# Optimization experiments

Measured on AMD Instinct MI355X. Metric: run time of the kernel, lower is better.

Reference implementation:

```python
import jax, jax.numpy as jnp
import numpy as np

K = 8                     # block_size
EPS_MIN, EPS_MAX = 2.0, 15.0
ROUND_M, ROUND_N = 10, 10
TEMP = 50.0               # round_temperature
INIT_QUALITY = 90

STD_LUMA = np.array([[16,11,10,16,24,40,51,61],[12,12,14,19,26,58,60,55],[14,13,16,24,40,57,69,56],[14,17,22,29,51,87,80,62],[18,22,37,56,68,109,103,77],[24,35,55,64,81,104,113,92],[49,64,78,87,103,121,120,101],[72,92,95,98,112,100,103,99]], dtype=np.float32)
STD_CHROMA = np.array([[17,18,24,47,99,99,99,99],[18,21,26,66,99,99,99,99],[24,26,56,99,99,99,99,99],[47,66,99,99,99,99,99,99],[99,99,99,99,99,99,99,99],[99,99,99,99,99,99,99,99],[99,99,99,99,99,99,99,99],[99,99,99,99,99,99,99,99]], dtype=np.float32)

def _quality_to_table(base, quality):
    scale = 5000.0 / quality if quality < 50 else 200.0 - 2.0 * quality
    return np.clip(np.floor((base * scale + 50.0) / 100.0), 1.0, 255.0).astype(np.float32)

def _dct_matrix(k):
    n = np.arange(k)
    mat = np.sqrt(2.0 / k) * np.cos((2 * n[None, :] + 1) * n[:, None] * np.pi / (2.0 * k))
    mat[0, :] = np.sqrt(1.0 / k)
    return jnp.asarray(mat, dtype=jnp.float32)

DCT = _dct_matrix(K)  # (K, K)

def _soft_round(x):
    # Differentiable staircase round over integer range [-M, N]:
    # round(x) ~= -M + sum_{k=-M}^{N-1} sigmoid(T * (x - k - 0.5))
    ks = jnp.arange(-ROUND_M, ROUND_N, dtype=jnp.float32)
    return -float(ROUND_M) + jnp.sum(jax.nn.sigmoid(TEMP * (x[..., None] - ks - 0.5)), axis=-1)

def setup_inputs() -> dict:
    key = jax.random.key(0)
    k_img, _ = jax.random.split(key)
    images = jax.random.uniform(k_img, (8, 3, 512, 512), dtype=jnp.float32)
    q_y = jnp.asarray(_quality_to_table(STD_LUMA, INIT_QUALITY))
    q_c = jnp.asarray(_quality_to_table(STD_CHROMA, INIT_QUALITY))
    return {"images": images, "q_y": q_y, "q_c": q_c}

def reference(images, q_y, q_c):
    x = jnp.clip(images, 0.0, 1.0)
    B, C, H, W = x.shape  # H, W are multiples of K (no padding needed)
    # RGB -> YCbCr
    r, g, b = x[:, 0:1], x[:, 1:2], x[:, 2:3]
    y  =  0.299 * r + 0.587 * g + 0.114 * b
    cb = -0.168736 * r - 0.331264 * g + 0.5 * b + 0.5
    cr =  0.5 * r - 0.418688 * g - 0.081312 * b + 0.5
    yc = jnp.concatenate([y, cb, cr], axis=1)
    # blockwise layout: (B, C, H/K, W/K, K, K)
    blocks = yc.reshape(B, C, H // K, K, W // K, K).transpose(0, 1, 2, 4, 3, 5)
    # 2D DCT per original code convention: coef = D @ X @ D (note: NOT D X D^T)
    coef = jnp.einsum('ij,bcuvjk,kl->bcuvil', DCT, blocks, DCT)
    # clamped learnable quant tables; chroma table shared by Cb and Cr
    qy = jnp.clip(q_y, EPS_MIN, EPS_MAX)
    qc = jnp.clip(q_c, EPS_MIN, EPS_MAX)
    qt = jnp.stack([qy, qc, qc])[None, :, None, None]  # (1,3,1,1,K,K)
    quant = _soft_round(coef / qt) * qt
    # 2D IDCT: rec = D^T @ X @ D^T (inverse of the above convention)
    rec = jnp.einsum('ji,bcuvjk,lk->bcuvil', DCT, quant, DCT)
    rec = rec.transpose(0, 1, 2, 4, 3, 5).reshape(B, C, H, W)
    # YCbCr -> RGB
    y2, cb2, cr2 = rec[:, 0:1], rec[:, 1:2] - 0.5, rec[:, 2:3] - 0.5
    r2 = y2 + 1.402 * cr2
    g2 = y2 - 0.344136 * cb2 - 0.714136 * cr2
    b2 = y2 + 1.772 * cb2
    out = jnp.concatenate([r2, g2, b2], axis=1)
    return jnp.clip(out, 0.0, 1.0)
```

## Files before the change

### kernel.cpp

```cpp
#include <hip/hip_runtime.h>
#include <math.h>

namespace {

constexpr int LDSS = 76;

struct DctMat {
  float d[8][8];
  constexpr DctMat() : d{} {
    const float CT[17] = {
        1.0f, 0.9807852804032304f, 0.9238795325112867f, 0.8314696123025452f,
        0.7071067811865476f, 0.5555702330196022f, 0.3826834323650898f,
        0.19509032201612825f, 0.0f, -0.19509032201612825f,
        -0.3826834323650898f, -0.5555702330196022f, -0.7071067811865476f,
        -0.8314696123025452f, -0.9238795325112867f, -0.9807852804032304f,
        -1.0f};
    for (int i = 0; i < 8; ++i)
      for (int j = 0; j < 8; ++j) {
        if (i == 0) {
          d[i][j] = 0.35355339059327373f;
        } else {
          int m = ((2 * j + 1) * i) % 32;
          if (m > 16) m = 32 - m;
          d[i][j] = 0.5f * CT[m];
        }
      }
  }
};
constexpr DctMat DM{};

template <bool TRANSPOSED>
__device__ __forceinline__ void mul8(const float (&a)[8], float (&t)[8]) {
#pragma unroll
  for (int i = 0; i < 8; ++i) {
    float s = 0.0f;
#pragma unroll
    for (int j = 0; j < 8; ++j) {
      s = fmaf(a[j], TRANSPOSED ? DM.d[j][i] : DM.d[i][j], s);
    }
    t[i] = s;
  }
}

__device__ __forceinline__ void transpose3(float (&T)[3][8], float* lds, int blk,
                                           int r) {
#pragma unroll
  for (int c = 0; c < 3; ++c) {
    float* lp = lds + (c * 8 + blk) * LDSS;
#pragma unroll
    for (int j = 0; j < 8; ++j) lp[j * 8 + r] = T[c][j];
  }
  __syncthreads();
#pragma unroll
  for (int c = 0; c < 3; ++c) {
    const float* lp = lds + (c * 8 + blk) * LDSS + r * 8;
    float4 v0 = *reinterpret_cast<const float4*>(lp);
    float4 v1 = *reinterpret_cast<const float4*>(lp + 4);
    T[c][0] = v0.x; T[c][1] = v0.y; T[c][2] = v0.z; T[c][3] = v0.w;
    T[c][4] = v1.x; T[c][5] = v1.y; T[c][6] = v1.z; T[c][7] = v1.w;
  }
  __syncthreads();
}

__device__ __forceinline__ void quant8(float (&a)[8], const float (&q)[8]) {
#pragma unroll
  for (int i = 0; i < 8; ++i) {
    float qv = q[i];
    float x = a[i] * __builtin_amdgcn_rcpf(qv);
    float kc = floorf(x);
    kc = fmaxf(-10.0f, fminf(9.0f, kc));
    float arg = 50.0f * (x - kc - 0.5f);
    float e = __expf(-arg);
    float sr = kc + __builtin_amdgcn_rcpf(1.0f + e);
    a[i] = sr * qv;
  }
}

__device__ __forceinline__ void load8(const float* __restrict__ p, float (&a)[8]) {
  float4 v0 = *reinterpret_cast<const float4*>(p);
  float4 v1 = *reinterpret_cast<const float4*>(p + 4);
  a[0] = v0.x; a[1] = v0.y; a[2] = v0.z; a[3] = v0.w;
  a[4] = v1.x; a[5] = v1.y; a[6] = v1.z; a[7] = v1.w;
}

__device__ __forceinline__ void store8(float* __restrict__ p, const float (&a)[8]) {
  float4 v0 = {a[0], a[1], a[2], a[3]};
  float4 v1 = {a[4], a[5], a[6], a[7]};
  *reinterpret_cast<float4*>(p) = v0;
  *reinterpret_cast<float4*>(p + 4) = v1;
}

__global__ __launch_bounds__(64) void jpeg_kernel(
    const float* __restrict__ img, const float* __restrict__ qy,
    const float* __restrict__ qc, float* __restrict__ out) {
  __shared__ float lds[3 * 8 * LDSS];

  const int lane = threadIdx.x;
  const int blk = lane & 7;
  const int r = lane >> 3;

  const int w = blockIdx.x;
  const int b = w >> 9;
  const int rr = w & 511;
  const int u = rr >> 3;
  const int v0 = (rr & 7) << 3;

  const int row = u * 8 + r;
  const int col = (v0 + blk) * 8;

  const size_t ims = 512 * 512;
  const float* pbase = img + (size_t)b * 3 * ims + (size_t)row * 512 + col;

  float R[8], G[8], B[8];
  load8(pbase, R);
  load8(pbase + ims, G);
  load8(pbase + 2 * ims, B);

  float qycol[8], qccol[8];
#pragma unroll
  for (int i = 0; i < 8; ++i) {
    qycol[i] = fminf(fmaxf(qy[i * 8 + r], 2.0f), 15.0f);
    qccol[i] = fminf(fmaxf(qc[i * 8 + r], 2.0f), 15.0f);
  }

  float A[3][8];
#pragma unroll
  for (int i = 0; i < 8; ++i) {
    float rv = fminf(fmaxf(R[i], 0.0f), 1.0f);
    float gv = fminf(fmaxf(G[i], 0.0f), 1.0f);
    float bv = fminf(fmaxf(B[i], 0.0f), 1.0f);
    A[0][i] = 0.299f * rv + 0.587f * gv + 0.114f * bv;
    A[1][i] = -0.168736f * rv - 0.331264f * gv + 0.5f * bv + 0.5f;
    A[2][i] = 0.5f * rv - 0.418688f * gv - 0.081312f * bv + 0.5f;
  }

  float T[3][8];
#pragma unroll
  for (int c = 0; c < 3; ++c) mul8<true>(A[c], T[c]);
  transpose3(T, lds, blk, r);
#pragma unroll
  for (int c = 0; c < 3; ++c) mul8<false>(T[c], A[c]);

  quant8(A[0], qycol);
  quant8(A[1], qccol);
  quant8(A[2], qccol);

#pragma unroll
  for (int c = 0; c < 3; ++c) mul8<true>(A[c], T[c]);
  transpose3(T, lds, blk, r);
#pragma unroll
  for (int c = 0; c < 3; ++c) mul8<false>(T[c], A[c]);

  float R2[8], G2[8], B2[8];
#pragma unroll
  for (int i = 0; i < 8; ++i) {
    float y2 = A[0][i];
    float cb2 = A[1][i] - 0.5f;
    float cr2 = A[2][i] - 0.5f;
    float r2 = y2 + 1.402f * cr2;
    float g2 = y2 - 0.344136f * cb2 - 0.714136f * cr2;
    float b2 = y2 + 1.772f * cb2;
    R2[i] = fminf(fmaxf(r2, 0.0f), 1.0f);
    G2[i] = fminf(fmaxf(g2, 0.0f), 1.0f);
    B2[i] = fminf(fmaxf(b2, 0.0f), 1.0f);
  }

  float* obase = out + (size_t)b * 3 * ims + (size_t)row * 512 + col;
  store8(obase, R2);
  store8(obase + ims, G2);
  store8(obase + 2 * ims, B2);
}

}

extern "C" void kernel_launch(void* const* d_in, const int* in_sizes, int n_in,
                              void* d_out, int out_size, void* d_ws, size_t ws_size,
                              hipStream_t stream) {
  const float* img = (const float*)d_in[0];
  const float* qy = (const float*)d_in[1];
  const float* qc = (const float*)d_in[2];
  float* out = (float*)d_out;
  jpeg_kernel<<<dim3(4096), dim3(64), 0, stream>>>(img, qy, qc, out);
}
```

Baseline: 81.98 us.

## Use butterfly DCT/IDCT, process two block strips per workgroup, precompute reciprocals

Replaces the dense 8x8 matrix-vector DCT passes with even/odd butterfly factorizations, cutting the multiply-adds per 8-point transform roughly in half. Each 64-thread workgroup now issues loads for two 64-column strips up front and processes them in turn, which halves the grid and gives more memory-level parallelism per wave. It also hoists the quant-table reciprocals out of the per-coefficient loop and folds the sigmoid scale into a single exp2. The cost is higher register pressure from holding two strips of data and fewer workgroups in flight.

```diff
diff --git a/kernel.cpp b/kernel.cpp
--- a/kernel.cpp
+++ b/kernel.cpp
@@ -5,41 +5,40 @@
 
 constexpr int LDSS = 76;
 
-struct DctMat {
-  float d[8][8];
-  constexpr DctMat() : d{} {
-    const float CT[17] = {
-        1.0f, 0.9807852804032304f, 0.9238795325112867f, 0.8314696123025452f,
-        0.7071067811865476f, 0.5555702330196022f, 0.3826834323650898f,
-        0.19509032201612825f, 0.0f, -0.19509032201612825f,
-        -0.3826834323650898f, -0.5555702330196022f, -0.7071067811865476f,
-        -0.8314696123025452f, -0.9238795325112867f, -0.9807852804032304f,
-        -1.0f};
-    for (int i = 0; i < 8; ++i)
-      for (int j = 0; j < 8; ++j) {
-        if (i == 0) {
-          d[i][j] = 0.35355339059327373f;
-        } else {
-          int m = ((2 * j + 1) * i) % 32;
-          if (m > 16) m = 32 - m;
-          d[i][j] = 0.5f * CT[m];
-        }
-      }
-  }
-};
-constexpr DctMat DM{};
+#define K0f 0.3535533905932738f
+#define K1f 0.4903926402016152f
+#define K2f 0.4619397662556434f
+#define K3f 0.4157348061512726f
+#define K5f 0.2777851165098011f
+#define K6f 0.1913417161825449f
+#define K7f 0.0975451610080642f
 
-template <bool TRANSPOSED>
-__device__ __forceinline__ void mul8(const float (&a)[8], float (&t)[8]) {
-#pragma unroll
-  for (int i = 0; i < 8; ++i) {
-    float s = 0.0f;
-#pragma unroll
-    for (int j = 0; j < 8; ++j) {
-      s = fmaf(a[j], TRANSPOSED ? DM.d[j][i] : DM.d[i][j], s);
-    }
-    t[i] = s;
-  }
+__device__ __forceinline__ void fdct8(const float (&x)[8], float (&t)[8]) {
+  float s0 = x[0] + x[7], s1 = x[1] + x[6], s2 = x[2] + x[5], s3 = x[3] + x[4];
+  float d0 = x[0] - x[7], d1 = x[1] - x[6], d2 = x[2] - x[5], d3 = x[3] - x[4];
+  float ss0 = s0 + s3, ss1 = s1 + s2, ds0 = s0 - s3, ds1 = s1 - s2;
+  t[0] = K0f * (ss0 + ss1);
+  t[4] = K0f * (ss0 - ss1);
+  t[2] = fmaf(K2f, ds0, K6f * ds1);
+  t[6] = fmaf(K6f, ds0, -K2f * ds1);
+  t[1] = fmaf(K1f, d0, fmaf(K3f, d1, fmaf(K5f, d2, K7f * d3)));
+  t[3] = fmaf(K3f, d0, fmaf(-K7f, d1, fmaf(-K1f, d2, -K5f * d3)));
+  t[5] = fmaf(K5f, d0, fmaf(-K1f, d1, fmaf(K7f, d2, K3f * d3)));
+  t[7] = fmaf(K7f, d0, fmaf(-K5f, d1, fmaf(K3f, d2, -K1f * d3)));
+}
+
+__device__ __forceinline__ void idct8(const float (&x)[8], float (&t)[8]) {
+  float ea = K0f * (x[0] + x[4]);
+  float eb = K0f * (x[0] - x[4]);
+  float ec = fmaf(K2f, x[2], K6f * x[6]);
+  float ed = fmaf(K6f, x[2], -K2f * x[6]);
+  float e0 = ea + ec, e1 = eb + ed, e2 = eb - ed, e3 = ea - ec;
+  float o0 = fmaf(K1f, x[1], fmaf(K3f, x[3], fmaf(K5f, x[5], K7f * x[7])));
+  float o1 = fmaf(K3f, x[1], fmaf(-K7f, x[3], fmaf(-K1f, x[5], -K5f * x[7])));
+  float o2 = fmaf(K5f, x[1], fmaf(-K1f, x[3], fmaf(K7f, x[5], K3f * x[7])));
+  float o3 = fmaf(K7f, x[1], fmaf(-K5f, x[3], fmaf(K3f, x[5], -K1f * x[7])));
+  t[0] = e0 + o0; t[1] = e1 + o1; t[2] = e2 + o2; t[3] = e3 + o3;
+  t[4] = e3 - o3; t[5] = e2 - o2; t[6] = e1 - o1; t[7] = e0 - o0;
 }
 
 __device__ __forceinline__ void transpose3(float (&T)[3][8], float* lds, int blk,
@@ -62,20 +61,6 @@
   __syncthreads();
 }
 
-__device__ __forceinline__ void quant8(float (&a)[8], const float (&q)[8]) {
-#pragma unroll
-  for (int i = 0; i < 8; ++i) {
-    float qv = q[i];
-    float x = a[i] * __builtin_amdgcn_rcpf(qv);
-    float kc = floorf(x);
-    kc = fmaxf(-10.0f, fminf(9.0f, kc));
-    float arg = 50.0f * (x - kc - 0.5f);
-    float e = __expf(-arg);
-    float sr = kc + __builtin_amdgcn_rcpf(1.0f + e);
-    a[i] = sr * qv;
-  }
-}
-
 __device__ __forceinline__ void load8(const float* __restrict__ p, float (&a)[8]) {
   float4 v0 = *reinterpret_cast<const float4*>(p);
   float4 v1 = *reinterpret_cast<const float4*>(p + 4);
@@ -90,6 +75,59 @@
   *reinterpret_cast<float4*>(p + 4) = v1;
 }
 
+__device__ __forceinline__ void process_strip(float (&R)[8], float (&G)[8],
+                                              float (&B)[8],
+                                              const float (&qv)[2][8],
+                                              const float (&qr)[2][8], float* lds,
+                                              int blk, int r) {
+  float A[3][8], T[3][8];
+#pragma unroll
+  for (int i = 0; i < 8; ++i) {
+    float rv = fminf(fmaxf(R[i], 0.0f), 1.0f);
+    float gv = fminf(fmaxf(G[i], 0.0f), 1.0f);
+    float bv = fminf(fmaxf(B[i], 0.0f), 1.0f);
+    A[0][i] = 0.299f * rv + 0.587f * gv + 0.114f * bv;
+    A[1][i] = -0.168736f * rv - 0.331264f * gv + 0.5f * bv + 0.5f;
+    A[2][i] = 0.5f * rv - 0.418688f * gv - 0.081312f * bv + 0.5f;
+  }
+#pragma unroll
+  for (int c = 0; c < 3; ++c) idct8(A[c], T[c]);
+  transpose3(T, lds, blk, r);
+#pragma unroll
+  for (int c = 0; c < 3; ++c) fdct8(T[c], A[c]);
+#pragma unroll
+  for (int c = 0; c < 3; ++c) {
+    const int ci = (c > 0);
+#pragma unroll
+    for (int i = 0; i < 8; ++i) {
+      float x = A[c][i] * qr[ci][i];
+      float kc = floorf(x);
+      kc = fmaxf(-10.0f, fminf(9.0f, kc));
+      float z = x - kc - 0.5f;
+      float e = __builtin_amdgcn_exp2f(-72.13475204444817f * z);
+      float sr = kc + __builtin_amdgcn_rcpf(1.0f + e);
+      A[c][i] = sr * qv[ci][i];
+    }
+  }
+#pragma unroll
+  for (int c = 0; c < 3; ++c) idct8(A[c], T[c]);
+  transpose3(T, lds, blk, r);
+#pragma unroll
+  for (int c = 0; c < 3; ++c) fdct8(T[c], A[c]);
+#pragma unroll
+  for (int i = 0; i < 8; ++i) {
+    float y2 = A[0][i];
+    float cb2 = A[1][i] - 0.5f;
+    float cr2 = A[2][i] - 0.5f;
+    float r2 = y2 + 1.402f * cr2;
+    float g2 = y2 - 0.344136f * cb2 - 0.714136f * cr2;
+    float b2 = y2 + 1.772f * cb2;
+    R[i] = fminf(fmaxf(r2, 0.0f), 1.0f);
+    G[i] = fminf(fmaxf(g2, 0.0f), 1.0f);
+    B[i] = fminf(fmaxf(b2, 0.0f), 1.0f);
+  }
+}
+
 __global__ __launch_bounds__(64) void jpeg_kernel(
     const float* __restrict__ img, const float* __restrict__ qy,
     const float* __restrict__ qc, float* __restrict__ out) {
@@ -99,76 +137,47 @@
   const int blk = lane & 7;
   const int r = lane >> 3;
 
-  const int w = blockIdx.x;
-  const int b = w >> 9;
-  const int rr = w & 511;
-  const int u = rr >> 3;
-  const int v0 = (rr & 7) << 3;
+  const int t = blockIdx.x;
+  const int b = t >> 8;
+  const int rr = t & 255;
+  const int u = rr >> 2;
+  const int p = rr & 3;
 
   const int row = u * 8 + r;
-  const int col = (v0 + blk) * 8;
+  const int colA = p * 128 + blk * 8;
 
   const size_t ims = 512 * 512;
-  const float* pbase = img + (size_t)b * 3 * ims + (size_t)row * 512 + col;
+  const float* pA = img + (size_t)b * 3 * ims + (size_t)row * 512 + colA;
+  const float* pB = pA + 64;
 
-  float R[8], G[8], B[8];
-  load8(pbase, R);
-  load8(pbase + ims, G);
-  load8(pbase + 2 * ims, B);
+  float RA[8], GA[8], BA[8], RB[8], GB[8], BB[8];
+  load8(pA, RA);
+  load8(pA + ims, GA);
+  load8(pA + 2 * ims, BA);
+  load8(pB, RB);
+  load8(pB + ims, GB);
+  load8(pB + 2 * ims, BB);
 
-  float qycol[8], qccol[8];
+  float qv[2][8], qr[2][8];
 #pragma unroll
   for (int i = 0; i < 8; ++i) {
-    qycol[i] = fminf(fmaxf(qy[i * 8 + r], 2.0f), 15.0f);
-    qccol[i] = fminf(fmaxf(qc[i * 8 + r], 2.0f), 15.0f);
+    qv[0][i] = fminf(fmaxf(qy[i * 8 + r], 2.0f), 15.0f);
+    qv[1][i] = fminf(fmaxf(qc[i * 8 + r], 2.0f), 15.0f);
+    qr[0][i] = __builtin_amdgcn_rcpf(qv[0][i]);
+    qr[1][i] = __builtin_amdgcn_rcpf(qv[1][i]);
   }
 
-  float A[3][8];
-#pragma unroll
-  for (int i = 0; i < 8; ++i) {
-    float rv = fminf(fmaxf(R[i], 0.0f), 1.0f);
-    float gv = fminf(fmaxf(G[i], 0.0f), 1.0f);
-    float bv = fminf(fmaxf(B[i], 0.0f), 1.0f);
-    A[0][i] = 0.299f * rv + 0.587f * gv + 0.114f * bv;
-    A[1][i] = -0.168736f * rv - 0.331264f * gv + 0.5f * bv + 0.5f;
-    A[2][i] = 0.5f * rv - 0.418688f * gv - 0.081312f * bv + 0.5f;
-  }
+  float* oA = out + (size_t)b * 3 * ims + (size_t)row * 512 + colA;
 
-  float T[3][8];
-#pragma unroll
-  for (int c = 0; c < 3; ++c) mul8<true>(A[c], T[c]);
-  transpose3(T, lds, blk, r);
-#pragma unroll
-  for (int c = 0; c < 3; ++c) mul8<false>(T[c], A[c]);
+  process_strip(RA, GA, BA, qv, qr, lds, blk, r);
+  store8(oA, RA);
+  store8(oA + ims, GA);
+  store8(oA + 2 * ims, BA);
 
-  quant8(A[0], qycol);
-  quant8(A[1], qccol);
-  quant8(A[2], qccol);
-
-#pragma unroll
-  for (int c = 0; c < 3; ++c) mul8<true>(A[c], T[c]);
-  transpose3(T, lds, blk, r);
-#pragma unroll
-  for (int c = 0; c < 3; ++c) mul8<false>(T[c], A[c]);
-
-  float R2[8], G2[8], B2[8];
-#pragma unroll
-  for (int i = 0; i < 8; ++i) {
-    float y2 = A[0][i];
-    float cb2 = A[1][i] - 0.5f;
-    float cr2 = A[2][i] - 0.5f;
-    float r2 = y2 + 1.402f * cr2;
-    float g2 = y2 - 0.344136f * cb2 - 0.714136f * cr2;
-    float b2 = y2 + 1.772f * cb2;
-    R2[i] = fminf(fmaxf(r2, 0.0f), 1.0f);
-    G2[i] = fminf(fmaxf(g2, 0.0f), 1.0f);
-    B2[i] = fminf(fmaxf(b2, 0.0f), 1.0f);
-  }
-
-  float* obase = out + (size_t)b * 3 * ims + (size_t)row * 512 + col;
-  store8(obase, R2);
-  store8(obase + ims, G2);
-  store8(obase + 2 * ims, B2);
+  process_strip(RB, GB, BB, qv, qr, lds, blk, r);
+  store8(oA + 64, RB);
+  store8(oA + 64 + ims, GB);
+  store8(oA + 64 + 2 * ims, BB);
 }
 
 }
@@ -180,5 +189,5 @@
   const float* qy = (const float*)d_in[1];
   const float* qc = (const float*)d_in[2];
   float* out = (float*)d_out;
-  jpeg_kernel<<<dim3(4096), dim3(64), 0, stream>>>(img, qy, qc, out);
+  jpeg_kernel<<<dim3(2048), dim3(64), 0, stream>>>(img, qy, qc, out);
 }
```

Measured after the change: 82.85 us. Within noise of the previous version (+1.1%).
